# Optimization experiments

Hardware: AMD Instinct MI355X
Metric: run time of the kernel (lower is better)

The kernel has to match this reference:

```python
import jax, jax.numpy as jnp
import numpy as np

N_NODES = 50000
N_HEDGES = 10000
NNZ_INC = 400000
NNZ_E = 80000
NNZ_V = 400000
VDIM = 128
EDIM = 128
OUT_VDIM = 128
OUT_EDIM = 128


def _spmm(rows, cols, vals, X, n_rows):
    # sparse COO [n_rows, n_cols] @ X  -> [n_rows, d]
    return jax.ops.segment_sum(vals[:, None] * X[cols], rows, num_segments=n_rows)


def setup_inputs() -> dict:
    key = jax.random.key(0)
    ks = jax.random.split(key, 20)
    inp = {
        "vfeat": jax.random.normal(ks[0], (N_NODES, VDIM), jnp.float32),
        "efeat": jax.random.normal(ks[1], (N_HEDGES, EDIM), jnp.float32),
        "invDV": jax.random.uniform(ks[2], (N_NODES,), jnp.float32),
        "invDE": jax.random.uniform(ks[3], (N_HEDGES,), jnp.float32),
        "inc_src": jax.random.randint(ks[4], (NNZ_INC,), 0, N_NODES, jnp.int32),
        "inc_dst": jax.random.randint(ks[5], (NNZ_INC,), 0, N_HEDGES, jnp.int32),
        "emat_rows": jax.random.randint(ks[6], (NNZ_E,), 0, N_HEDGES, jnp.int32),
        "emat_cols": jax.random.randint(ks[7], (NNZ_E,), 0, N_HEDGES, jnp.int32),
        "emat_vals": jax.random.normal(ks[8], (NNZ_E,), jnp.float32),
        "vmat_rows": jax.random.randint(ks[9], (NNZ_V,), 0, N_NODES, jnp.int32),
        "vmat_cols": jax.random.randint(ks[10], (NNZ_V,), 0, N_NODES, jnp.int32),
        "vmat_vals": jax.random.normal(ks[11], (NNZ_V,), jnp.float32),
        # parameters (torch Linear: y = x @ W.T + b)
        "Wv": jax.random.normal(ks[12], (OUT_VDIM, VDIM), jnp.float32) * 0.05,
        "We": jax.random.normal(ks[13], (OUT_EDIM, EDIM), jnp.float32) * 0.05,
        "psi1_W": jax.random.normal(ks[14], (VDIM, VDIM + EDIM), jnp.float32) * 0.05,
        "psi1_b": jnp.zeros((VDIM,), jnp.float32),
        "psi2_W": jax.random.normal(ks[15], (EDIM, OUT_VDIM + EDIM), jnp.float32) * 0.05,
        "psi2_b": jnp.zeros((EDIM,), jnp.float32),
    }
    return inp


def reference(vfeat, efeat, invDV, invDE, inc_src, inc_dst,
              emat_rows, emat_cols, emat_vals,
              vmat_rows, vmat_cols, vmat_vals,
              Wv, We, psi1_W, psi1_b, psi2_W, psi2_b):
    N = vfeat.shape[0]
    E = efeat.shape[0]
    # --- 'in' update_all with psi1: per-incidence concat -> linear -> *invDV[src] -> sum into hyperedge
    x = jnp.concatenate([vfeat[inc_src], efeat[inc_dst]], axis=1)  # [nnz, VDIM+EDIM]
    x = x @ psi1_W.T + psi1_b                                       # [nnz, VDIM]
    x = x * invDV[inc_src][:, None]
    A = jax.ops.segment_sum(x, inc_dst, num_segments=E)             # [E, VDIM]
    A = _spmm(emat_rows, emat_cols, emat_vals, A, E)
    _efeat = A + efeat
    # --- 'con' update_all: node gathers sum of incident hyperedge feats
    _vfeat = jax.ops.segment_sum(_efeat[inc_dst], inc_src, num_segments=N)
    vfeat_out = jax.nn.relu(_vfeat @ Wv.T)                           # [N, OUT_VDIM]
    # --- 'in' update_all with psi2 (dv = ones)
    x2 = jnp.concatenate([vfeat_out[inc_src], efeat[inc_dst]], axis=1)
    x2 = x2 @ psi2_W.T + psi2_b                                      # [nnz, EDIM]
    B = jax.ops.segment_sum(x2, inc_dst, num_segments=E) * invDE[:, None]
    # --- 'con' pass with efeat, then vMat spmm, then 'in' sum back to hyperedges
    _vfeat2 = jax.ops.segment_sum(efeat[inc_dst], inc_src, num_segments=N)
    _vfeat2 = _spmm(vmat_rows, vmat_cols, vmat_vals, _vfeat2, N)
    _efeat2 = jax.ops.segment_sum(_vfeat2[inc_src], inc_dst, num_segments=E)
    _efeat2 = _efeat2 + B
    efeat_out = jax.nn.relu(_efeat2 @ We.T)                          # [E, OUT_EDIM]
    return vfeat_out, efeat_out
```

## Files before the change

kernel.cpp:

```cpp
#include <hip/hip_runtime.h>

#define NN 50000
#define NE 10000
#define NNZ_INC 400000
#define NNZ_E 80000
#define NNZ_V 400000
#define D 128
#define KC 32

#define CAP_D 112
#define CAP_S 40
#define CAP_E 40
#define CAP_V 40

#define GN_ 782
#define GE_ 157
#define G_HINC ((NNZ_INC + 255) / 256)
#define G_EV ((NNZ_E + NNZ_V + 255) / 256)
#define G_CVTN 6250
#define G_CVTE 1250
#define GNR (NN / 4)
#define GER (NE / 4)

typedef unsigned short u16;
typedef unsigned int u32;

__device__ __forceinline__ u16 f2bf(float x) {
    unsigned u = __float_as_uint(x);
    unsigned r = u + 0x7fffu + ((u >> 16) & 1u);
    return (u16)(r >> 16);
}
__device__ __forceinline__ float bf2f(u16 h) {
    return __uint_as_float(((unsigned)h) << 16);
}
__device__ __forceinline__ float2 ldbf2(const u16* rowbase, int l) {
    ushort2 t = ((const ushort2*)rowbase)[l];
    return make_float2(bf2f(t.x), bf2f(t.y));
}

__device__ __forceinline__ void gemm_acc(
    int bx, const float* __restrict__ X, const float* __restrict__ W, int ldw,
    int M, float acc[8][4])
{
    __shared__ float XsT[KC][68];
    __shared__ float Ws[KC][132];
    const int tid = threadIdx.x;
    const int tx = tid & 31, ty = tid >> 5;
    const int row0 = bx * 64;
    const int c0 = tx * 4;
    const int r0 = ty * 8;

#pragma unroll
    for (int r = 0; r < 8; ++r)
#pragma unroll
        for (int c = 0; c < 4; ++c) acc[r][c] = 0.f;

    for (int kc = 0; kc < D; kc += KC) {
        __syncthreads();
#pragma unroll
        for (int it = 0; it < 2; ++it) {
            int l = tid + it * 256;
            int r = l >> 3, k4 = l & 7;
            float4 v = make_float4(0.f, 0.f, 0.f, 0.f);
            int row = row0 + r;
            if (row < M) v = ((const float4*)(X + (size_t)row * D + kc))[k4];
            int k = k4 * 4;
            XsT[k + 0][r] = v.x; XsT[k + 1][r] = v.y;
            XsT[k + 2][r] = v.z; XsT[k + 3][r] = v.w;
        }
#pragma unroll
        for (int it = 0; it < 4; ++it) {
            int l = tid + it * 256;
            int o = l >> 3, k4 = l & 7;
            float4 w = ((const float4*)(W + (size_t)o * ldw + kc))[k4];
            int k = k4 * 4;
            Ws[k + 0][o] = w.x; Ws[k + 1][o] = w.y;
            Ws[k + 2][o] = w.z; Ws[k + 3][o] = w.w;
        }
        __syncthreads();
#pragma unroll
        for (int k = 0; k < KC; ++k) {
            const float4 a0 = *(const float4*)&XsT[k][r0];
            const float4 a1 = *(const float4*)&XsT[k][r0 + 4];
            const float4 b  = *(const float4*)&Ws[k][c0];
            float av[8] = {a0.x, a0.y, a0.z, a0.w, a1.x, a1.y, a1.z, a1.w};
            float bv[4] = {b.x, b.y, b.z, b.w};
#pragma unroll
            for (int r = 0; r < 8; ++r)
#pragma unroll
                for (int c = 0; c < 4; ++c)
                    acc[r][c] = fmaf(av[r], bv[c], acc[r][c]);
        }
    }
}

__global__ __launch_bounds__(256) void mega0(
    const int* __restrict__ inc_src, const int* __restrict__ inc_dst,
    int* __restrict__ cnt_dst, int* __restrict__ cnt_src,
    u16* __restrict__ ell_d, u16* __restrict__ ell_s,
    const float* __restrict__ efeat, const float* __restrict__ vfeat,
    const float* __restrict__ invDV,
    const float* __restrict__ psi1_W, const float* __restrict__ psi1_b, float* __restrict__ PeP,
    const float* __restrict__ psi2_W, const float* __restrict__ psi2_b, float* __restrict__ QeP,
    u16* __restrict__ vfi_b, u16* __restrict__ efeat_b)
{
    int b = blockIdx.x;
    if (b < G_HINC) {
        int i = b * 256 + threadIdx.x;
        if (i < NNZ_INC) {
            int s = inc_src[i], d = inc_dst[i];
            int rd = atomicAdd(cnt_dst + d, 1);
            if (rd < CAP_D) ell_d[d * CAP_D + rd] = (u16)s;
            int rs = atomicAdd(cnt_src + s, 1);
            if (rs < CAP_S) ell_s[s * CAP_S + rs] = (u16)d;
        }
    } else if (b < G_HINC + 2 * GE_) {
        int lb = b - G_HINC;
        const float* Wp = (lb < GE_) ? psi1_W + D : psi2_W + D;
        const float* bp = (lb < GE_) ? psi1_b : psi2_b;
        float* outp     = (lb < GE_) ? PeP : QeP;
        int bx = (lb < GE_) ? lb : lb - GE_;
        float acc[8][4];
        gemm_acc(bx, efeat, Wp, 2 * D, NE, acc);
        int tx = threadIdx.x & 31, ty = threadIdx.x >> 5;
        float4 b4 = ((const float4*)bp)[tx];
#pragma unroll
        for (int r = 0; r < 8; ++r) {
            int row = bx * 64 + ty * 8 + r;
            if (row < NE) {
                float4 v = make_float4(acc[r][0] + b4.x, acc[r][1] + b4.y,
                                       acc[r][2] + b4.z, acc[r][3] + b4.w);
                ((float4*)(outp + (size_t)row * D))[tx] = v;
            }
        }
    } else if (b < G_HINC + 2 * GE_ + G_CVTN) {
        int i = ((b - G_HINC - 2 * GE_) * 256 + threadIdx.x) * 4;
        int row = i >> 7;
        float s = invDV[row];
        float4 v = *(const float4*)(vfeat + i);
        ushort4 u;
        u.x = f2bf(v.x * s); u.y = f2bf(v.y * s);
        u.z = f2bf(v.z * s); u.w = f2bf(v.w * s);
        *(ushort4*)(vfi_b + i) = u;
    } else {
        int i = ((b - G_HINC - 2 * GE_ - G_CVTN) * 256 + threadIdx.x) * 4;
        float4 v = *(const float4*)(efeat + i);
        ushort4 u;
        u.x = f2bf(v.x); u.y = f2bf(v.y); u.z = f2bf(v.z); u.w = f2bf(v.w);
        *(ushort4*)(efeat_b + i) = u;
    }
}

__device__ __forceinline__ void segsum_bf_ell(int rb,
    const int* __restrict__ cnt, int cap, const u16* __restrict__ ell,
    const u16* __restrict__ Tb, u16* __restrict__ Yb, int R)
{
    int r = rb * 4 + (threadIdx.x >> 6);
    int l = threadIdx.x & 63;
    if (r >= R) return;
    int m = min(cnt[r], cap);
    const u16* lst = ell + (size_t)r * cap;
    float2 acc = make_float2(0.f, 0.f);
    int j = 0;
    for (; j + 3 < m; j += 4) {
        int d0 = lst[j], d1 = lst[j+1], d2 = lst[j+2], d3 = lst[j+3];
        float2 p0 = ldbf2(Tb + (size_t)d0 * D, l);
        float2 p1 = ldbf2(Tb + (size_t)d1 * D, l);
        float2 p2 = ldbf2(Tb + (size_t)d2 * D, l);
        float2 p3 = ldbf2(Tb + (size_t)d3 * D, l);
        acc.x += (p0.x + p1.x) + (p2.x + p3.x);
        acc.y += (p0.y + p1.y) + (p2.y + p3.y);
    }
    for (; j < m; ++j) {
        float2 p = ldbf2(Tb + (size_t)lst[j] * D, l);
        acc.x += p.x; acc.y += p.y;
    }
    ushort2 u; u.x = f2bf(acc.x); u.y = f2bf(acc.y);
    ((ushort2*)(Yb + (size_t)r * D))[l] = u;
}

__device__ __forceinline__ void segsum_f_ell(int rb,
    const int* __restrict__ cnt, int cap, const u16* __restrict__ ell,
    const u16* __restrict__ Tb, float* __restrict__ Y, int R)
{
    int r = rb * 4 + (threadIdx.x >> 6);
    int l = threadIdx.x & 63;
    if (r >= R) return;
    int m = min(cnt[r], cap);
    const u16* lst = ell + (size_t)r * cap;
    float2 acc = make_float2(0.f, 0.f);
    int j = 0;
    for (; j + 3 < m; j += 4) {
        int d0 = lst[j], d1 = lst[j+1], d2 = lst[j+2], d3 = lst[j+3];
        float2 p0 = ldbf2(Tb + (size_t)d0 * D, l);
        float2 p1 = ldbf2(Tb + (size_t)d1 * D, l);
        float2 p2 = ldbf2(Tb + (size_t)d2 * D, l);
        float2 p3 = ldbf2(Tb + (size_t)d3 * D, l);
        acc.x += (p0.x + p1.x) + (p2.x + p3.x);
        acc.y += (p0.y + p1.y) + (p2.y + p3.y);
    }
    for (; j < m; ++j) {
        float2 p = ldbf2(Tb + (size_t)lst[j] * D, l);
        acc.x += p.x; acc.y += p.y;
    }
    ((float2*)(Y + (size_t)r * D))[l] = acc;
}

__device__ __forceinline__ void spmm_bf_ell(int rb,
    const int* __restrict__ cnt, int cap, const u32* __restrict__ ell,
    const u16* __restrict__ Xb, const float* __restrict__ addend,
    u16* __restrict__ Yb, int R)
{
    int r = rb * 4 + (threadIdx.x >> 6);
    int l = threadIdx.x & 63;
    if (r >= R) return;
    int m = min(cnt[r], cap);
    const u32* lst = ell + (size_t)r * cap;
    float2 acc = addend ? ((const float2*)(addend + (size_t)r * D))[l]
                        : make_float2(0.f, 0.f);
    int j = 0;
    for (; j + 3 < m; j += 4) {
        u32 e0 = lst[j], e1 = lst[j+1], e2 = lst[j+2], e3 = lst[j+3];
        float2 x0 = ldbf2(Xb + (size_t)(e0 >> 16) * D, l);
        float2 x1 = ldbf2(Xb + (size_t)(e1 >> 16) * D, l);
        float2 x2 = ldbf2(Xb + (size_t)(e2 >> 16) * D, l);
        float2 x3 = ldbf2(Xb + (size_t)(e3 >> 16) * D, l);
        float v0 = bf2f((u16)e0), v1 = bf2f((u16)e1);
        float v2 = bf2f((u16)e2), v3 = bf2f((u16)e3);
        acc.x = fmaf(v0, x0.x, fmaf(v1, x1.x, fmaf(v2, x2.x, fmaf(v3, x3.x, acc.x))));
        acc.y = fmaf(v0, x0.y, fmaf(v1, x1.y, fmaf(v2, x2.y, fmaf(v3, x3.y, acc.y))));
    }
    for (; j < m; ++j) {
        u32 e = lst[j];
        float2 x = ldbf2(Xb + (size_t)(e >> 16) * D, l);
        float v = bf2f((u16)e);
        acc.x = fmaf(v, x.x, acc.x);
        acc.y = fmaf(v, x.y, acc.y);
    }
    ushort2 u; u.x = f2bf(acc.x); u.y = f2bf(acc.y);
    ((ushort2*)(Yb + (size_t)r * D))[l] = u;
}

__global__ __launch_bounds__(256) void fusedA(
    const int* __restrict__ erows, const int* __restrict__ ecols,
    const float* __restrict__ evals, int* __restrict__ cnt_e, u32* __restrict__ ev_e,
    const int* __restrict__ vrows, const int* __restrict__ vcols,
    const float* __restrict__ vvals, int* __restrict__ cnt_v, u32* __restrict__ ev_v,
    const int* __restrict__ cnt_dst, const u16* __restrict__ ell_d,
    const float* __restrict__ invDV, const u16* __restrict__ vfi_b,
    float* __restrict__ sva, float* __restrict__ wsum,
    const int* __restrict__ cnt_src, const u16* __restrict__ ell_s,
    const u16* __restrict__ efeat_b, u16* __restrict__ vf2_b)
{
    int b = blockIdx.x;
    if (b < G_EV) {
        int i = b * 256 + threadIdx.x;
        if (i < NNZ_E) {
            int r = erows[i];
            int re = atomicAdd(cnt_e + r, 1);
            if (re < CAP_E)
                ev_e[r * CAP_E + re] = ((u32)ecols[i] << 16) | (u32)f2bf(evals[i]);
        } else if (i < NNZ_E + NNZ_V) {
            int j = i - NNZ_E;
            int r = vrows[j];
            int rv = atomicAdd(cnt_v + r, 1);
            if (rv < CAP_V)
                ev_v[r * CAP_V + rv] = ((u32)vcols[j] << 16) | (u32)f2bf(vvals[j]);
        }
    } else if (b < G_EV + GER) {
        int e = (b - G_EV) * 4 + (threadIdx.x >> 6);
        int l = threadIdx.x & 63;
        if (e >= NE) return;
        int m = min(cnt_dst[e], CAP_D);
        const u16* lst = ell_d + (size_t)e * CAP_D;
        float2 acc = make_float2(0.f, 0.f);
        float ws = 0.f;
        int j = 0;
        for (; j + 3 < m; j += 4) {
            int s0 = lst[j], s1 = lst[j+1], s2 = lst[j+2], s3 = lst[j+3];
            float2 p0 = ldbf2(vfi_b + (size_t)s0 * D, l);
            float2 p1 = ldbf2(vfi_b + (size_t)s1 * D, l);
            float2 p2 = ldbf2(vfi_b + (size_t)s2 * D, l);
            float2 p3 = ldbf2(vfi_b + (size_t)s3 * D, l);
            ws += (invDV[s0] + invDV[s1]) + (invDV[s2] + invDV[s3]);
            acc.x += (p0.x + p1.x) + (p2.x + p3.x);
            acc.y += (p0.y + p1.y) + (p2.y + p3.y);
        }
        for (; j < m; ++j) {
            int s = lst[j];
            float2 p = ldbf2(vfi_b + (size_t)s * D, l);
            ws += invDV[s];
            acc.x += p.x; acc.y += p.y;
        }
        ((float2*)(sva + (size_t)e * D))[l] = acc;
        if (l == 0) wsum[e] = ws;
    } else {
        segsum_bf_ell(b - G_EV - GER, cnt_src, CAP_S, ell_s, efeat_b, vf2_b, NN);
    }
}

__global__ __launch_bounds__(256) void gemmA_k(
    const float* __restrict__ sva, const float* __restrict__ psi1_W,
    const float* __restrict__ wsum, const float* __restrict__ PeP,
    u16* __restrict__ A_b)
{
    float acc[8][4];
    gemm_acc(blockIdx.x, sva, psi1_W, 2 * D, NE, acc);
    int tx = threadIdx.x & 31, ty = threadIdx.x >> 5;
#pragma unroll
    for (int r = 0; r < 8; ++r) {
        int row = blockIdx.x * 64 + ty * 8 + r;
        if (row < NE) {
            float ws = wsum[row];
            float4 pe = ((const float4*)(PeP + (size_t)row * D))[tx];
            ushort4 u;
            u.x = f2bf(fmaf(ws, pe.x, acc[r][0]));
            u.y = f2bf(fmaf(ws, pe.y, acc[r][1]));
            u.z = f2bf(fmaf(ws, pe.z, acc[r][2]));
            u.w = f2bf(fmaf(ws, pe.w, acc[r][3]));
            ((ushort4*)(A_b + (size_t)row * D))[tx] = u;
        }
    }
}

__global__ __launch_bounds__(256) void fusedB(
    const int* __restrict__ cnt_e, const u32* __restrict__ ev_e,
    const u16* __restrict__ A_b, const float* __restrict__ efeat, u16* __restrict__ A2_b,
    const int* __restrict__ cnt_v, const u32* __restrict__ ev_v,
    const u16* __restrict__ vf2_b, u16* __restrict__ vf2b_b)
{
    int b = blockIdx.x;
    if (b < GER) spmm_bf_ell(b, cnt_e, CAP_E, ev_e, A_b, efeat, A2_b, NE);
    else spmm_bf_ell(b - GER, cnt_v, CAP_V, ev_v, vf2_b, nullptr, vf2b_b, NN);
}

__global__ __launch_bounds__(256) void fusedD(
    const int* __restrict__ cnt_src, const u16* __restrict__ ell_s,
    const u16* __restrict__ A2_b, float* __restrict__ vf1,
    const int* __restrict__ cnt_dst, const u16* __restrict__ ell_d,
    const u16* __restrict__ vf2b_b, float* __restrict__ av)
{
    int b = blockIdx.x;
    if (b < GNR) segsum_f_ell(b, cnt_src, CAP_S, ell_s, A2_b, vf1, NN);
    else segsum_f_ell(b - GNR, cnt_dst, CAP_D, ell_d, vf2b_b, av, NE);
}

__global__ __launch_bounds__(256) void gemmC_k(
    const float* __restrict__ vf1, const float* __restrict__ Wv,
    float* __restrict__ out_v, u16* __restrict__ outv_b)
{
    float acc[8][4];
    gemm_acc(blockIdx.x, vf1, Wv, D, NN, acc);
    int tx = threadIdx.x & 31, ty = threadIdx.x >> 5;
#pragma unroll
    for (int r = 0; r < 8; ++r) {
        int row = blockIdx.x * 64 + ty * 8 + r;
        if (row < NN) {
            float4 v = make_float4(fmaxf(acc[r][0], 0.f), fmaxf(acc[r][1], 0.f),
                                   fmaxf(acc[r][2], 0.f), fmaxf(acc[r][3], 0.f));
            ((float4*)(out_v + (size_t)row * D))[tx] = v;
            ushort4 u;
            u.x = f2bf(v.x); u.y = f2bf(v.y); u.z = f2bf(v.z); u.w = f2bf(v.w);
            ((ushort4*)(outv_b + (size_t)row * D))[tx] = u;
        }
    }
}

__global__ __launch_bounds__(256) void gather_sv(
    const int* __restrict__ cnt_dst, const u16* __restrict__ ell_d,
    const u16* __restrict__ outv_b, float* __restrict__ sv)
{
    segsum_f_ell(blockIdx.x, cnt_dst, CAP_D, ell_d, outv_b, sv, NE);
}

__global__ __launch_bounds__(256) void gemmBE_k(
    const float* __restrict__ sv, const float* __restrict__ psi2_W,
    const int* __restrict__ cnt_dst, const float* __restrict__ QeP,
    const float* __restrict__ invDE, const float* __restrict__ av,
    const float* __restrict__ We, float* __restrict__ out_e)
{
    __shared__ float T[D][68];
    float acc[8][4];
    gemm_acc(blockIdx.x, sv, psi2_W, 2 * D, NE, acc);
    const int tx = threadIdx.x & 31, ty = threadIdx.x >> 5;
    const int bx = blockIdx.x;
#pragma unroll
    for (int r = 0; r < 8; ++r) {
        int row = bx * 64 + ty * 8 + r;
        float deg = 0.f, ide = 0.f;
        float4 qe = make_float4(0.f, 0.f, 0.f, 0.f);
        float4 a  = make_float4(0.f, 0.f, 0.f, 0.f);
        if (row < NE) {
            deg = (float)cnt_dst[row];
            ide = invDE[row];
            qe = ((const float4*)(QeP + (size_t)row * D))[tx];
            a  = ((const float4*)(av  + (size_t)row * D))[tx];
        }
        int lr = ty * 8 + r;
        T[tx * 4 + 0][lr] = fmaf(deg, qe.x, acc[r][0]) * ide + a.x;
        T[tx * 4 + 1][lr] = fmaf(deg, qe.y, acc[r][1]) * ide + a.y;
        T[tx * 4 + 2][lr] = fmaf(deg, qe.z, acc[r][2]) * ide + a.z;
        T[tx * 4 + 3][lr] = fmaf(deg, qe.w, acc[r][3]) * ide + a.w;
    }
    __shared__ float Ws2[KC][132];
    float acc2[8][4];
#pragma unroll
    for (int r = 0; r < 8; ++r)
#pragma unroll
        for (int c = 0; c < 4; ++c) acc2[r][c] = 0.f;
    const int c0 = tx * 4, r0 = ty * 8;
    for (int kc = 0; kc < D; kc += KC) {
        __syncthreads();
#pragma unroll
        for (int it = 0; it < 4; ++it) {
            int l = threadIdx.x + it * 256;
            int o = l >> 3, k4 = l & 7;
            float4 w = ((const float4*)(We + (size_t)o * D + kc))[k4];
            int k = k4 * 4;
            Ws2[k + 0][o] = w.x; Ws2[k + 1][o] = w.y;
            Ws2[k + 2][o] = w.z; Ws2[k + 3][o] = w.w;
        }
        __syncthreads();
#pragma unroll
        for (int k = 0; k < KC; ++k) {
            const float4 a0 = *(const float4*)&T[kc + k][r0];
            const float4 a1 = *(const float4*)&T[kc + k][r0 + 4];
            const float4 bb = *(const float4*)&Ws2[k][c0];
            float avv[8] = {a0.x, a0.y, a0.z, a0.w, a1.x, a1.y, a1.z, a1.w};
            float bv[4] = {bb.x, bb.y, bb.z, bb.w};
#pragma unroll
            for (int r = 0; r < 8; ++r)
#pragma unroll
                for (int c = 0; c < 4; ++c)
                    acc2[r][c] = fmaf(avv[r], bv[c], acc2[r][c]);
        }
    }
#pragma unroll
    for (int r = 0; r < 8; ++r) {
        int row = bx * 64 + ty * 8 + r;
        if (row < NE) {
            float4 v = make_float4(fmaxf(acc2[r][0], 0.f), fmaxf(acc2[r][1], 0.f),
                                   fmaxf(acc2[r][2], 0.f), fmaxf(acc2[r][3], 0.f));
            ((float4*)(out_e + (size_t)row * D))[tx] = v;
        }
    }
}

extern "C" void kernel_launch(void* const* d_in, const int* in_sizes, int n_in,
                              void* d_out, int out_size, void* d_ws, size_t ws_size,
                              hipStream_t stream)
{
    (void)in_sizes; (void)n_in; (void)out_size; (void)ws_size;
    const float* vfeat     = (const float*)d_in[0];
    const float* efeat     = (const float*)d_in[1];
    const float* invDV     = (const float*)d_in[2];
    const float* invDE     = (const float*)d_in[3];
    const int*   inc_src   = (const int*)d_in[4];
    const int*   inc_dst   = (const int*)d_in[5];
    const int*   emat_rows = (const int*)d_in[6];
    const int*   emat_cols = (const int*)d_in[7];
    const float* emat_vals = (const float*)d_in[8];
    const int*   vmat_rows = (const int*)d_in[9];
    const int*   vmat_cols = (const int*)d_in[10];
    const float* vmat_vals = (const float*)d_in[11];
    const float* Wv        = (const float*)d_in[12];
    const float* We        = (const float*)d_in[13];
    const float* psi1_W    = (const float*)d_in[14];
    const float* psi1_b    = (const float*)d_in[15];
    const float* psi2_W    = (const float*)d_in[16];
    const float* psi2_b    = (const float*)d_in[17];

    const size_t ND = (size_t)NN * D;
    const size_t ED = (size_t)NE * D;

    char* p = (char*)d_ws;
    auto alloc = [&](size_t bytes) {
        size_t a = (size_t)p; a = (a + 15) & ~(size_t)15;
        p = (char*)a; void* r = (void*)p; p += bytes; return r;
    };
    float* PeP   = (float*)alloc(ED * 4);
    float* QeP   = (float*)alloc(ED * 4);
    float* vf1   = (float*)alloc(ND * 4);
    float* av    = (float*)alloc(ED * 4);
    float* svbuf = (float*)alloc(ED * 4);
    float* wsum  = (float*)alloc((size_t)NE * 4);
    u16* vfi_b   = (u16*)alloc(ND * 2);
    u16* outv_b  = (u16*)alloc(ND * 2);
    u16* vf2_b   = (u16*)alloc(ND * 2);
    u16* vf2b_b  = (u16*)alloc(ND * 2);
    u16* efeat_b = (u16*)alloc(ED * 2);
    u16* A_b     = (u16*)alloc(ED * 2);
    u16* A2_b    = (u16*)alloc(ED * 2);
    int* cnt_dst = (int*)alloc((size_t)(2 * NE + 2 * NN) * 4);
    int* cnt_src = cnt_dst + NE;
    int* cnt_e   = cnt_src + NN;
    int* cnt_v   = cnt_e + NE;
    u16* ell_d   = (u16*)alloc((size_t)NE * CAP_D * 2);
    u16* ell_s   = (u16*)alloc((size_t)NN * CAP_S * 2);
    u32* ev_e    = (u32*)alloc((size_t)NE * CAP_E * 4);
    u32* ev_v    = (u32*)alloc((size_t)NN * CAP_V * 4);

    float* out_v = (float*)d_out;
    float* out_e = out_v + ND;

    dim3 b256(256);

    hipMemsetAsync(cnt_dst, 0, (size_t)(2 * NE + 2 * NN) * sizeof(int), stream);
    mega0<<<G_HINC + 2 * GE_ + G_CVTN + G_CVTE, b256, 0, stream>>>(
        inc_src, inc_dst, cnt_dst, cnt_src, ell_d, ell_s,
        efeat, vfeat, invDV,
        psi1_W, psi1_b, PeP, psi2_W, psi2_b, QeP, vfi_b, efeat_b);
    fusedA<<<G_EV + GER + GNR, b256, 0, stream>>>(
        emat_rows, emat_cols, emat_vals, cnt_e, ev_e,
        vmat_rows, vmat_cols, vmat_vals, cnt_v, ev_v,
        cnt_dst, ell_d, invDV, vfi_b, svbuf, wsum,
        cnt_src, ell_s, efeat_b, vf2_b);
    gemmA_k<<<GE_, b256, 0, stream>>>(svbuf, psi1_W, wsum, PeP, A_b);
    fusedB<<<GER + GNR, b256, 0, stream>>>(
        cnt_e, ev_e, A_b, efeat, A2_b,
        cnt_v, ev_v, vf2_b, vf2b_b);
    fusedD<<<GNR + GER, b256, 0, stream>>>(
        cnt_src, ell_s, A2_b, vf1,
        cnt_dst, ell_d, vf2b_b, av);
    gemmC_k<<<GN_, b256, 0, stream>>>(vf1, Wv, out_v, outv_b);
    gather_sv<<<GER, b256, 0, stream>>>(cnt_dst, ell_d, outv_b, svbuf);
    gemmBE_k<<<GE_, b256, 0, stream>>>(svbuf, psi2_W, cnt_dst, QeP, invDE, av, We, out_e);
}
```

Baseline: 400.3 us.

## Widen sparse gathers to 16-byte loads and pad atomic counters

All ELL gather and SpMM kernels now give 16 lanes to each row, each lane loading 8 bf16 values with a 16-byte vector load, so one block covers 16 rows instead of 4. Index lists are read as vector loads too. The per-row atomic counters are spaced 16 ints apart, so atomics on different rows no longer share a cache line, and workspace allocations are aligned to 256 bytes. In exchange, each lane keeps more accumulators in registers, and the padded counters need a 16x larger memset and more cache footprint.

```diff
diff --git a/kernel.cpp b/kernel.cpp
--- a/kernel.cpp
+++ b/kernel.cpp
@@ -13,14 +13,16 @@
 #define CAP_E 40
 #define CAP_V 40
 
+#define CSTR 16
+
 #define GN_ 782
 #define GE_ 157
 #define G_HINC ((NNZ_INC + 255) / 256)
 #define G_EV ((NNZ_E + NNZ_V + 255) / 256)
 #define G_CVTN 6250
 #define G_CVTE 1250
-#define GNR (NN / 4)
-#define GER (NE / 4)
+#define G_NR16 (NN / 16)
+#define G_ER16 (NE / 16)
 
 typedef unsigned short u16;
 typedef unsigned int u32;
@@ -33,9 +35,34 @@
 __device__ __forceinline__ float bf2f(u16 h) {
     return __uint_as_float(((unsigned)h) << 16);
 }
-__device__ __forceinline__ float2 ldbf2(const u16* rowbase, int l) {
-    ushort2 t = ((const ushort2*)rowbase)[l];
-    return make_float2(bf2f(t.x), bf2f(t.y));
+
+__device__ __forceinline__ void acc8(uint4 u, float acc[8]) {
+    acc[0] += __uint_as_float(u.x << 16);
+    acc[1] += __uint_as_float(u.x & 0xffff0000u);
+    acc[2] += __uint_as_float(u.y << 16);
+    acc[3] += __uint_as_float(u.y & 0xffff0000u);
+    acc[4] += __uint_as_float(u.z << 16);
+    acc[5] += __uint_as_float(u.z & 0xffff0000u);
+    acc[6] += __uint_as_float(u.w << 16);
+    acc[7] += __uint_as_float(u.w & 0xffff0000u);
+}
+__device__ __forceinline__ void fma8(uint4 u, float v, float acc[8]) {
+    acc[0] = fmaf(v, __uint_as_float(u.x << 16), acc[0]);
+    acc[1] = fmaf(v, __uint_as_float(u.x & 0xffff0000u), acc[1]);
+    acc[2] = fmaf(v, __uint_as_float(u.y << 16), acc[2]);
+    acc[3] = fmaf(v, __uint_as_float(u.y & 0xffff0000u), acc[3]);
+    acc[4] = fmaf(v, __uint_as_float(u.z << 16), acc[4]);
+    acc[5] = fmaf(v, __uint_as_float(u.z & 0xffff0000u), acc[5]);
+    acc[6] = fmaf(v, __uint_as_float(u.w << 16), acc[6]);
+    acc[7] = fmaf(v, __uint_as_float(u.w & 0xffff0000u), acc[7]);
+}
+__device__ __forceinline__ uint4 pack_bf8(const float acc[8]) {
+    uint4 o;
+    o.x = (u32)f2bf(acc[0]) | ((u32)f2bf(acc[1]) << 16);
+    o.y = (u32)f2bf(acc[2]) | ((u32)f2bf(acc[3]) << 16);
+    o.z = (u32)f2bf(acc[4]) | ((u32)f2bf(acc[5]) << 16);
+    o.w = (u32)f2bf(acc[6]) | ((u32)f2bf(acc[7]) << 16);
+    return o;
 }
 
 __device__ __forceinline__ void gemm_acc(
@@ -109,9 +136,9 @@
         int i = b * 256 + threadIdx.x;
         if (i < NNZ_INC) {
             int s = inc_src[i], d = inc_dst[i];
-            int rd = atomicAdd(cnt_dst + d, 1);
+            int rd = atomicAdd(cnt_dst + (size_t)d * CSTR, 1);
             if (rd < CAP_D) ell_d[d * CAP_D + rd] = (u16)s;
-            int rs = atomicAdd(cnt_src + s, 1);
+            int rs = atomicAdd(cnt_src + (size_t)s * CSTR, 1);
             if (rs < CAP_S) ell_s[s * CAP_S + rs] = (u16)d;
         }
     } else if (b < G_HINC + 2 * GE_) {
@@ -151,94 +178,99 @@
     }
 }
 
-__device__ __forceinline__ void segsum_bf_ell(int rb,
+__device__ __forceinline__ void segsum_bf_ell16(int rb,
     const int* __restrict__ cnt, int cap, const u16* __restrict__ ell,
     const u16* __restrict__ Tb, u16* __restrict__ Yb, int R)
 {
-    int r = rb * 4 + (threadIdx.x >> 6);
-    int l = threadIdx.x & 63;
+    int r = rb * 16 + (threadIdx.x >> 4);
+    int q = threadIdx.x & 15;
     if (r >= R) return;
-    int m = min(cnt[r], cap);
+    int m = min(cnt[(size_t)r * CSTR], cap);
     const u16* lst = ell + (size_t)r * cap;
-    float2 acc = make_float2(0.f, 0.f);
+    float acc[8] = {0.f, 0.f, 0.f, 0.f, 0.f, 0.f, 0.f, 0.f};
     int j = 0;
     for (; j + 3 < m; j += 4) {
-        int d0 = lst[j], d1 = lst[j+1], d2 = lst[j+2], d3 = lst[j+3];
-        float2 p0 = ldbf2(Tb + (size_t)d0 * D, l);
-        float2 p1 = ldbf2(Tb + (size_t)d1 * D, l);
-        float2 p2 = ldbf2(Tb + (size_t)d2 * D, l);
-        float2 p3 = ldbf2(Tb + (size_t)d3 * D, l);
-        acc.x += (p0.x + p1.x) + (p2.x + p3.x);
-        acc.y += (p0.y + p1.y) + (p2.y + p3.y);
+        ushort4 ix = *(const ushort4*)(lst + j);
+        uint4 u0 = *(const uint4*)(Tb + (size_t)ix.x * D + q * 8);
+        uint4 u1 = *(const uint4*)(Tb + (size_t)ix.y * D + q * 8);
+        uint4 u2 = *(const uint4*)(Tb + (size_t)ix.z * D + q * 8);
+        uint4 u3 = *(const uint4*)(Tb + (size_t)ix.w * D + q * 8);
+        acc8(u0, acc); acc8(u1, acc); acc8(u2, acc); acc8(u3, acc);
     }
     for (; j < m; ++j) {
-        float2 p = ldbf2(Tb + (size_t)lst[j] * D, l);
-        acc.x += p.x; acc.y += p.y;
-    }
-    ushort2 u; u.x = f2bf(acc.x); u.y = f2bf(acc.y);
-    ((ushort2*)(Yb + (size_t)r * D))[l] = u;
-}
-
-__device__ __forceinline__ void segsum_f_ell(int rb,
+        uint4 u0 = *(const uint4*)(Tb + (size_t)lst[j] * D + q * 8);
+        acc8(u0, acc);
+    }
+    ((uint4*)(Yb + (size_t)r * D))[q] = pack_bf8(acc);
+}
+
+__device__ __forceinline__ void segsum_f_ell16(int rb,
     const int* __restrict__ cnt, int cap, const u16* __restrict__ ell,
     const u16* __restrict__ Tb, float* __restrict__ Y, int R)
 {
-    int r = rb * 4 + (threadIdx.x >> 6);
-    int l = threadIdx.x & 63;
+    int r = rb * 16 + (threadIdx.x >> 4);
+    int q = threadIdx.x & 15;
     if (r >= R) return;
-    int m = min(cnt[r], cap);
+    int m = min(cnt[(size_t)r * CSTR], cap);
     const u16* lst = ell + (size_t)r * cap;
-    float2 acc = make_float2(0.f, 0.f);
+    float acc[8] = {0.f, 0.f, 0.f, 0.f, 0.f, 0.f, 0.f, 0.f};
     int j = 0;
     for (; j + 3 < m; j += 4) {
-        int d0 = lst[j], d1 = lst[j+1], d2 = lst[j+2], d3 = lst[j+3];
-        float2 p0 = ldbf2(Tb + (size_t)d0 * D, l);
-        float2 p1 = ldbf2(Tb + (size_t)d1 * D, l);
-        float2 p2 = ldbf2(Tb + (size_t)d2 * D, l);
-        float2 p3 = ldbf2(Tb + (size_t)d3 * D, l);
-        acc.x += (p0.x + p1.x) + (p2.x + p3.x);
-        acc.y += (p0.y + p1.y) + (p2.y + p3.y);
+        ushort4 ix = *(const ushort4*)(lst + j);
+        uint4 u0 = *(const uint4*)(Tb + (size_t)ix.x * D + q * 8);
+        uint4 u1 = *(const uint4*)(Tb + (size_t)ix.y * D + q * 8);
+        uint4 u2 = *(const uint4*)(Tb + (size_t)ix.z * D + q * 8);
+        uint4 u3 = *(const uint4*)(Tb + (size_t)ix.w * D + q * 8);
+        acc8(u0, acc); acc8(u1, acc); acc8(u2, acc); acc8(u3, acc);
     }
     for (; j < m; ++j) {
-        float2 p = ldbf2(Tb + (size_t)lst[j] * D, l);
-        acc.x += p.x; acc.y += p.y;
-    }
-    ((float2*)(Y + (size_t)r * D))[l] = acc;
-}
-
-__device__ __forceinline__ void spmm_bf_ell(int rb,
+        uint4 u0 = *(const uint4*)(Tb + (size_t)lst[j] * D + q * 8);
+        acc8(u0, acc);
+    }
+    float* yr = Y + (size_t)r * D;
+    ((float4*)yr)[2 * q + 0] = make_float4(acc[0], acc[1], acc[2], acc[3]);
+    ((float4*)yr)[2 * q + 1] = make_float4(acc[4], acc[5], acc[6], acc[7]);
+}
+
+__device__ __forceinline__ void spmm_bf_ell16(int rb,
     const int* __restrict__ cnt, int cap, const u32* __restrict__ ell,
     const u16* __restrict__ Xb, const float* __restrict__ addend,
     u16* __restrict__ Yb, int R)
 {
-    int r = rb * 4 + (threadIdx.x >> 6);
-    int l = threadIdx.x & 63;
+    int r = rb * 16 + (threadIdx.x >> 4);
+    int q = threadIdx.x & 15;
     if (r >= R) return;
-    int m = min(cnt[r], cap);
+    int m = min(cnt[(size_t)r * CSTR], cap);
     const u32* lst = ell + (size_t)r * cap;
-    float2 acc = addend ? ((const float2*)(addend + (size_t)r * D))[l]
-                        : make_float2(0.f, 0.f);
+    float acc[8];
+    if (addend) {
+        const float* ar = addend + (size_t)r * D;
+        float4 lo = ((const float4*)ar)[2 * q + 0];
+        float4 hi = ((const float4*)ar)[2 * q + 1];
+        acc[0] = lo.x; acc[1] = lo.y; acc[2] = lo.z; acc[3] = lo.w;
+        acc[4] = hi.x; acc[5] = hi.y; acc[6] = hi.z; acc[7] = hi.w;
+    } else {
+#pragma unroll
+        for (int i = 0; i < 8; ++i) acc[i] = 0.f;
+    }
     int j = 0;
     for (; j + 3 < m; j += 4) {
-        u32 e0 = lst[j], e1 = lst[j+1], e2 = lst[j+2], e3 = lst[j+3];
-        float2 x0 = ldbf2(Xb + (size_t)(e0 >> 16) * D, l);
-        float2 x1 = ldbf2(Xb + (size_t)(e1 >> 16) * D, l);
-        float2 x2 = ldbf2(Xb + (size_t)(e2 >> 16) * D, l);
-        float2 x3 = ldbf2(Xb + (size_t)(e3 >> 16) * D, l);
-        float v0 = bf2f((u16)e0), v1 = bf2f((u16)e1);
-        float v2 = bf2f((u16)e2), v3 = bf2f((u16)e3);
-        acc.x = fmaf(v0, x0.x, fmaf(v1, x1.x, fmaf(v2, x2.x, fmaf(v3, x3.x, acc.x))));
-        acc.y = fmaf(v0, x0.y, fmaf(v1, x1.y, fmaf(v2, x2.y, fmaf(v3, x3.y, acc.y))));
+        uint4 e = *(const uint4*)(lst + j);
+        uint4 x0 = *(const uint4*)(Xb + (size_t)(e.x >> 16) * D + q * 8);
+        uint4 x1 = *(const uint4*)(Xb + (size_t)(e.y >> 16) * D + q * 8);
+        uint4 x2 = *(const uint4*)(Xb + (size_t)(e.z >> 16) * D + q * 8);
+        uint4 x3 = *(const uint4*)(Xb + (size_t)(e.w >> 16) * D + q * 8);
+        fma8(x0, __uint_as_float(e.x << 16), acc);
+        fma8(x1, __uint_as_float(e.y << 16), acc);
+        fma8(x2, __uint_as_float(e.z << 16), acc);
+        fma8(x3, __uint_as_float(e.w << 16), acc);
     }
     for (; j < m; ++j) {
         u32 e = lst[j];
-        float2 x = ldbf2(Xb + (size_t)(e >> 16) * D, l);
-        float v = bf2f((u16)e);
-        acc.x = fmaf(v, x.x, acc.x);
-        acc.y = fmaf(v, x.y, acc.y);
-    }
-    ushort2 u; u.x = f2bf(acc.x); u.y = f2bf(acc.y);
-    ((ushort2*)(Yb + (size_t)r * D))[l] = u;
+        uint4 x = *(const uint4*)(Xb + (size_t)(e >> 16) * D + q * 8);
+        fma8(x, __uint_as_float(e << 16), acc);
+    }
+    ((uint4*)(Yb + (size_t)r * D))[q] = pack_bf8(acc);
 }
 
 __global__ __launch_bounds__(256) void fusedA(
@@ -257,45 +289,46 @@
         int i = b * 256 + threadIdx.x;
         if (i < NNZ_E) {
             int r = erows[i];
-            int re = atomicAdd(cnt_e + r, 1);
+            int re = atomicAdd(cnt_e + (size_t)r * CSTR, 1);
             if (re < CAP_E)
                 ev_e[r * CAP_E + re] = ((u32)ecols[i] << 16) | (u32)f2bf(evals[i]);
         } else if (i < NNZ_E + NNZ_V) {
             int j = i - NNZ_E;
             int r = vrows[j];
-            int rv = atomicAdd(cnt_v + r, 1);
+            int rv = atomicAdd(cnt_v + (size_t)r * CSTR, 1);
             if (rv < CAP_V)
                 ev_v[r * CAP_V + rv] = ((u32)vcols[j] << 16) | (u32)f2bf(vvals[j]);
         }
-    } else if (b < G_EV + GER) {
-        int e = (b - G_EV) * 4 + (threadIdx.x >> 6);
-        int l = threadIdx.x & 63;
+    } else if (b < G_EV + G_ER16) {
+        int e = (b - G_EV) * 16 + (threadIdx.x >> 4);
+        int q = threadIdx.x & 15;
         if (e >= NE) return;
-        int m = min(cnt_dst[e], CAP_D);
+        int m = min(cnt_dst[(size_t)e * CSTR], CAP_D);
         const u16* lst = ell_d + (size_t)e * CAP_D;
-        float2 acc = make_float2(0.f, 0.f);
+        float acc[8] = {0.f, 0.f, 0.f, 0.f, 0.f, 0.f, 0.f, 0.f};
         float ws = 0.f;
         int j = 0;
         for (; j + 3 < m; j += 4) {
-            int s0 = lst[j], s1 = lst[j+1], s2 = lst[j+2], s3 = lst[j+3];
-            float2 p0 = ldbf2(vfi_b + (size_t)s0 * D, l);
-            float2 p1 = ldbf2(vfi_b + (size_t)s1 * D, l);
-            float2 p2 = ldbf2(vfi_b + (size_t)s2 * D, l);
-            float2 p3 = ldbf2(vfi_b + (size_t)s3 * D, l);
-            ws += (invDV[s0] + invDV[s1]) + (invDV[s2] + invDV[s3]);
-            acc.x += (p0.x + p1.x) + (p2.x + p3.x);
-            acc.y += (p0.y + p1.y) + (p2.y + p3.y);
+            ushort4 ix = *(const ushort4*)(lst + j);
+            uint4 u0 = *(const uint4*)(vfi_b + (size_t)ix.x * D + q * 8);
+            uint4 u1 = *(const uint4*)(vfi_b + (size_t)ix.y * D + q * 8);
+            uint4 u2 = *(const uint4*)(vfi_b + (size_t)ix.z * D + q * 8);
+            uint4 u3 = *(const uint4*)(vfi_b + (size_t)ix.w * D + q * 8);
+            ws += (invDV[ix.x] + invDV[ix.y]) + (invDV[ix.z] + invDV[ix.w]);
+            acc8(u0, acc); acc8(u1, acc); acc8(u2, acc); acc8(u3, acc);
         }
         for (; j < m; ++j) {
             int s = lst[j];
-            float2 p = ldbf2(vfi_b + (size_t)s * D, l);
+            uint4 u0 = *(const uint4*)(vfi_b + (size_t)s * D + q * 8);
             ws += invDV[s];
-            acc.x += p.x; acc.y += p.y;
-        }
-        ((float2*)(sva + (size_t)e * D))[l] = acc;
-        if (l == 0) wsum[e] = ws;
+            acc8(u0, acc);
+        }
+        float* yr = sva + (size_t)e * D;
+        ((float4*)yr)[2 * q + 0] = make_float4(acc[0], acc[1], acc[2], acc[3]);
+        ((float4*)yr)[2 * q + 1] = make_float4(acc[4], acc[5], acc[6], acc[7]);
+        if (q == 0) wsum[e] = ws;
     } else {
-        segsum_bf_ell(b - G_EV - GER, cnt_src, CAP_S, ell_s, efeat_b, vf2_b, NN);
+        segsum_bf_ell16(b - G_EV - G_ER16, cnt_src, CAP_S, ell_s, efeat_b, vf2_b, NN);
     }
 }
 
@@ -330,8 +363,8 @@
     const u16* __restrict__ vf2_b, u16* __restrict__ vf2b_b)
 {
     int b = blockIdx.x;
-    if (b < GER) spmm_bf_ell(b, cnt_e, CAP_E, ev_e, A_b, efeat, A2_b, NE);
-    else spmm_bf_ell(b - GER, cnt_v, CAP_V, ev_v, vf2_b, nullptr, vf2b_b, NN);
+    if (b < G_ER16) spmm_bf_ell16(b, cnt_e, CAP_E, ev_e, A_b, efeat, A2_b, NE);
+    else spmm_bf_ell16(b - G_ER16, cnt_v, CAP_V, ev_v, vf2_b, nullptr, vf2b_b, NN);
 }
 
 __global__ __launch_bounds__(256) void fusedD(
@@ -341,8 +374,8 @@
     const u16* __restrict__ vf2b_b, float* __restrict__ av)
 {
     int b = blockIdx.x;
-    if (b < GNR) segsum_f_ell(b, cnt_src, CAP_S, ell_s, A2_b, vf1, NN);
-    else segsum_f_ell(b - GNR, cnt_dst, CAP_D, ell_d, vf2b_b, av, NE);
+    if (b < G_NR16) segsum_f_ell16(b, cnt_src, CAP_S, ell_s, A2_b, vf1, NN);
+    else segsum_f_ell16(b - G_NR16, cnt_dst, CAP_D, ell_d, vf2b_b, av, NE);
 }
 
 __global__ __launch_bounds__(256) void gemmC_k(
@@ -370,7 +403,7 @@
     const int* __restrict__ cnt_dst, const u16* __restrict__ ell_d,
     const u16* __restrict__ outv_b, float* __restrict__ sv)
 {
-    segsum_f_ell(blockIdx.x, cnt_dst, CAP_D, ell_d, outv_b, sv, NE);
+    segsum_f_ell16(blockIdx.x, cnt_dst, CAP_D, ell_d, outv_b, sv, NE);
 }
 
 __global__ __launch_bounds__(256) void gemmBE_k(
@@ -391,7 +424,7 @@
         float4 qe = make_float4(0.f, 0.f, 0.f, 0.f);
         float4 a  = make_float4(0.f, 0.f, 0.f, 0.f);
         if (row < NE) {
-            deg = (float)cnt_dst[row];
+            deg = (float)cnt_dst[(size_t)row * CSTR];
             ide = invDE[row];
             qe = ((const float4*)(QeP + (size_t)row * D))[tx];
             a  = ((const float4*)(av  + (size_t)row * D))[tx];
@@ -475,7 +508,7 @@
 
     char* p = (char*)d_ws;
     auto alloc = [&](size_t bytes) {
-        size_t a = (size_t)p; a = (a + 15) & ~(size_t)15;
+        size_t a = (size_t)p; a = (a + 255) & ~(size_t)255;
         p = (char*)a; void* r = (void*)p; p += bytes; return r;
     };
     float* PeP   = (float*)alloc(ED * 4);
@@ -491,10 +524,10 @@
     u16* efeat_b = (u16*)alloc(ED * 2);
     u16* A_b     = (u16*)alloc(ED * 2);
     u16* A2_b    = (u16*)alloc(ED * 2);
-    int* cnt_dst = (int*)alloc((size_t)(2 * NE + 2 * NN) * 4);
-    int* cnt_src = cnt_dst + NE;
-    int* cnt_e   = cnt_src + NN;
-    int* cnt_v   = cnt_e + NE;
+    int* cnt_dst = (int*)alloc((size_t)(2 * NE + 2 * NN) * CSTR * 4);
+    int* cnt_src = cnt_dst + (size_t)NE * CSTR;
+    int* cnt_e   = cnt_src + (size_t)NN * CSTR;
+    int* cnt_v   = cnt_e + (size_t)NE * CSTR;
     u16* ell_d   = (u16*)alloc((size_t)NE * CAP_D * 2);
     u16* ell_s   = (u16*)alloc((size_t)NN * CAP_S * 2);
     u32* ev_e    = (u32*)alloc((size_t)NE * CAP_E * 4);
@@ -505,24 +538,24 @@
 
     dim3 b256(256);
 
-    hipMemsetAsync(cnt_dst, 0, (size_t)(2 * NE + 2 * NN) * sizeof(int), stream);
+    hipMemsetAsync(cnt_dst, 0, (size_t)(2 * NE + 2 * NN) * CSTR * sizeof(int), stream);
     mega0<<<G_HINC + 2 * GE_ + G_CVTN + G_CVTE, b256, 0, stream>>>(
         inc_src, inc_dst, cnt_dst, cnt_src, ell_d, ell_s,
         efeat, vfeat, invDV,
         psi1_W, psi1_b, PeP, psi2_W, psi2_b, QeP, vfi_b, efeat_b);
-    fusedA<<<G_EV + GER + GNR, b256, 0, stream>>>(
+    fusedA<<<G_EV + G_ER16 + G_NR16, b256, 0, stream>>>(
         emat_rows, emat_cols, emat_vals, cnt_e, ev_e,
         vmat_rows, vmat_cols, vmat_vals, cnt_v, ev_v,
         cnt_dst, ell_d, invDV, vfi_b, svbuf, wsum,
         cnt_src, ell_s, efeat_b, vf2_b);
     gemmA_k<<<GE_, b256, 0, stream>>>(svbuf, psi1_W, wsum, PeP, A_b);
-    fusedB<<<GER + GNR, b256, 0, stream>>>(
+    fusedB<<<G_ER16 + G_NR16, b256, 0, stream>>>(
         cnt_e, ev_e, A_b, efeat, A2_b,
         cnt_v, ev_v, vf2_b, vf2b_b);
-    fusedD<<<GNR + GER, b256, 0, stream>>>(
+    fusedD<<<G_NR16 + G_ER16, b256, 0, stream>>>(
         cnt_src, ell_s, A2_b, vf1,
         cnt_dst, ell_d, vf2b_b, av);
     gemmC_k<<<GN_, b256, 0, stream>>>(vf1, Wv, out_v, outv_b);
-    gather_sv<<<GER, b256, 0, stream>>>(cnt_dst, ell_d, outv_b, svbuf);
+    gather_sv<<<G_ER16, b256, 0, stream>>>(cnt_dst, ell_d, outv_b, svbuf);
     gemmBE_k<<<GE_, b256, 0, stream>>>(svbuf, psi2_W, cnt_dst, QeP, invDE, av, We, out_e);
 }
```

Result: faster. 365.4 us (-8.7%).
